# Performance work log

Measured on AMD Instinct MI355X. Metric: run time of the kernel, lower is better.

## Reference

```python
import jax, jax.numpy as jnp
import numpy as np

B, T, C = 2, 2048, 2048
N_HEAD, N_KV = 16, 2
D_HEAD = C // N_HEAD          # 128
R = N_HEAD // N_KV            # q heads per kv head = 8


def setup_inputs() -> dict:
    key = jax.random.key(0)
    ks = jax.random.split(key, 5)
    s = 0.02
    return {
        "x": jax.random.normal(ks[0], (B, T, C), dtype=jnp.float32),
        "Wq": jax.random.normal(ks[1], (C, C), dtype=jnp.float32) * s,
        "Wk": jax.random.normal(ks[2], (C, N_KV * D_HEAD), dtype=jnp.float32) * s,
        "Wv": jax.random.normal(ks[3], (C, N_KV * D_HEAD), dtype=jnp.float32) * s,
        "Wo": jax.random.normal(ks[4], (C, C), dtype=jnp.float32) * s,
    }


def reference(x, Wq, Wk, Wv, Wo):
    b, t, c = x.shape
    # projections (no bias per config.bias=False)
    q = (x @ Wq).reshape(b, t, N_KV, R, D_HEAD)        # group q heads by kv group
    k = (x @ Wk).reshape(b, t, N_KV, D_HEAD)
    v = (x @ Wv).reshape(b, t, N_KV, D_HEAD)
    scale = 1.0 / jnp.sqrt(jnp.float32(D_HEAD))
    # scores: [b, g(kv), r, tq, tk] -- broadcast kv heads instead of repeat_interleave
    att = jnp.einsum('btgrd,bsgd->bgrts', q, k) * scale
    causal = jnp.tril(jnp.ones((t, t), dtype=bool))
    att = jnp.where(causal, att, -jnp.inf)
    att = jax.nn.softmax(att, axis=-1)
    y = jnp.einsum('bgrts,bsgd->btgrd', att, v).reshape(b, t, c)
    return y @ Wo
```

## Files before the change

kernel.cpp:

```cpp
#include <hip/hip_runtime.h>
#include <stdint.h>

using bf16x8 = __attribute__((ext_vector_type(8))) __bf16;
using f32x4  = __attribute__((ext_vector_type(4))) float;

#define GLL(g, l) __builtin_amdgcn_global_load_lds(                                  \
    (const __attribute__((address_space(1))) void*)(g),                              \
    (__attribute__((address_space(3))) void*)(l), 16, 0, 0)

__device__ __forceinline__ unsigned short f2bf(float f) {
  unsigned u = __builtin_bit_cast(unsigned, f);
  u += 0x7FFF + ((u >> 16) & 1);
  return (unsigned short)(u >> 16);
}
__device__ __forceinline__ float bf2f(unsigned short u) {
  unsigned v = ((unsigned)u) << 16;
  return __builtin_bit_cast(float, v);
}

__global__ __launch_bounds__(256) void cast_kernel(const float* __restrict__ in,
                                                   unsigned short* __restrict__ out, int n4) {
  int i = blockIdx.x * 256 + threadIdx.x;
  if (i >= n4) return;
  float4 v = reinterpret_cast<const float4*>(in)[i];
  ushort4 o;
  o.x = f2bf(v.x); o.y = f2bf(v.y); o.z = f2bf(v.z); o.w = f2bf(v.w);
  reinterpret_cast<ushort4*>(out)[i] = o;
}

__global__ __launch_bounds__(256) void tcast_all_kernel(const float* __restrict__ Wq,
                                                        const float* __restrict__ Wk,
                                                        const float* __restrict__ Wv,
                                                        const float* __restrict__ Wo,
                                                        unsigned short* __restrict__ Wqkvt,
                                                        unsigned short* __restrict__ Wot) {
  __shared__ float T[64][65];
  const int y = blockIdx.y;
  const float* W;
  unsigned short* Wt;
  int N, n0;
  if (y < 32)      { W = Wq; Wt = Wqkvt;                          N = 2048; n0 = y * 64; }
  else if (y < 36) { W = Wk; Wt = Wqkvt + (size_t)2048 * 2048;    N = 256;  n0 = (y - 32) * 64; }
  else if (y < 40) { W = Wv; Wt = Wqkvt + (size_t)2304 * 2048;    N = 256;  n0 = (y - 36) * 64; }
  else             { W = Wo; Wt = Wot;                            N = 2048; n0 = (y - 40) * 64; }
  const int k0 = blockIdx.x * 64;
  const int t = threadIdx.x;
  const int r4 = t >> 6, c = t & 63;
#pragma unroll
  for (int p = 0; p < 16; ++p) {
    int r = p * 4 + r4;
    T[r][c] = W[(size_t)(k0 + r) * N + n0 + c];
  }
  __syncthreads();
#pragma unroll
  for (int p = 0; p < 16; ++p) {
    int r = p * 4 + r4;
    Wt[(size_t)(n0 + r) * 2048 + k0 + c] = f2bf(T[c][r]);
  }
}

__global__ __launch_bounds__(256) void tv_kernel(const unsigned short* __restrict__ V,
                                                 unsigned short* __restrict__ Vt) {
  __shared__ unsigned short T[64][68];
  const int t0 = blockIdx.x * 64;
  const int d0 = blockIdx.y * 64;
  const int t = threadIdx.x;
  const int r4 = t >> 6, c = t & 63;
#pragma unroll
  for (int p = 0; p < 16; ++p) {
    int r = p * 4 + r4;
    T[r][c] = V[(size_t)(t0 + r) * 2560 + 2304 + d0 + c];
  }
  __syncthreads();
  const int b = t0 >> 11;
  const int tl = t0 & 2047;
#pragma unroll
  for (int p = 0; p < 16; ++p) {
    int dr = p * 4 + r4;
    int dg = d0 + dr;
    int g = dg >> 7, dl = dg & 127;
    Vt[(size_t)((b * 2 + g) * 128 + dl) * 2048 + tl + c] = T[c][dr];
  }
}

template <bool FP32OUT>
__global__ __launch_bounds__(256) void gemm_bt_kernel(const unsigned short* __restrict__ A,
                                                      const unsigned short* __restrict__ Bt,
                                                      void* __restrict__ Cout,
                                                      int K, int lda, int ldb, int ldc,
                                                      float scale, int nscale) {
  __shared__ __align__(16) unsigned short As[128 * 64];
  __shared__ __align__(16) unsigned short Bs[128 * 64];
  const int m0 = blockIdx.x * 128, n0 = blockIdx.y * 128;
  const int t = threadIdx.x;
  const int w = t >> 6, lane = t & 63;
  const int l15 = lane & 15, quad = lane >> 4;
  const int wm = (w >> 1) * 64, wn = (w & 1) * 64;

  const int srow = lane >> 3;
  const int sgl = (lane & 7) ^ srow;

  f32x4 acc[4][4] = {};

  for (int k0 = 0; k0 < K; k0 += 64) {
    __syncthreads();
#pragma unroll
    for (int p = 0; p < 4; ++p) {
      int rowbase = p * 32 + w * 8;
      GLL(&A[(size_t)(m0 + rowbase + srow) * lda + k0 + sgl * 8], &As[rowbase * 64]);
      GLL(&Bt[(size_t)(n0 + rowbase + srow) * ldb + k0 + sgl * 8], &Bs[rowbase * 64]);
    }
    __syncthreads();
#pragma unroll
    for (int kk = 0; kk < 64; kk += 32) {
      const int kg = kk >> 3;
      const int phys = ((kg + quad) ^ (l15 & 7)) * 8;
      bf16x8 af[4], bfr[4];
#pragma unroll
      for (int mt = 0; mt < 4; ++mt)
        af[mt] = *reinterpret_cast<const bf16x8*>(&As[(wm + mt * 16 + l15) * 64 + phys]);
#pragma unroll
      for (int nt = 0; nt < 4; ++nt)
        bfr[nt] = *reinterpret_cast<const bf16x8*>(&Bs[(wn + nt * 16 + l15) * 64 + phys]);
#pragma unroll
      for (int mt = 0; mt < 4; ++mt)
#pragma unroll
        for (int nt = 0; nt < 4; ++nt)
          acc[mt][nt] = __builtin_amdgcn_mfma_f32_16x16x32_bf16(af[mt], bfr[nt], acc[mt][nt], 0, 0, 0);
    }
  }

  const float sc = (n0 < nscale) ? scale : 1.0f;
#pragma unroll
  for (int mt = 0; mt < 4; ++mt) {
#pragma unroll
    for (int reg = 0; reg < 4; ++reg) {
      int row = m0 + wm + mt * 16 + quad * 4 + reg;
#pragma unroll
      for (int nt = 0; nt < 4; ++nt) {
        int col = n0 + wn + nt * 16 + l15;
        float v = acc[mt][nt][reg] * sc;
        if (FP32OUT)
          reinterpret_cast<float*>(Cout)[(size_t)row * ldc + col] = v;
        else
          reinterpret_cast<unsigned short*>(Cout)[(size_t)row * ldc + col] = f2bf(v);
      }
    }
  }
}

#define LDQK 2560
__global__ __launch_bounds__(256, 4) void attn_kernel(const unsigned short* __restrict__ Q,
                                                      const unsigned short* __restrict__ Kg,
                                                      const unsigned short* __restrict__ Vt,
                                                      float* __restrict__ O0,
                                                      unsigned short* __restrict__ O1,
                                                      float* __restrict__ L) {
  __shared__ __align__(16) unsigned short Ks[2][32 * 128];
  __shared__ __align__(16) unsigned short Vs[2][128 * 32];
  __shared__ __align__(16) unsigned short Pw[4][16 * 40];

  const int s  = blockIdx.x;
  const int by = blockIdx.y;
  const int hh = blockIdx.z & 15;
  const int b  = blockIdx.z >> 4;
  const int g  = hh >> 3;
  const int t  = threadIdx.x;
  const int wg = t >> 6, lane = t & 63;
  const int l15 = lane & 15, quad = lane >> 4;

  const unsigned short* Kbase = Kg + (size_t)b * 2048 * LDQK + g * 128;
  const unsigned short* Vbase = Vt + (size_t)(b * 2 + g) * 128 * 2048;

  const int k_r = lane >> 4;
  const int k_g = lane & 15;
  const int v_r = lane >> 2;
  const int v_g = lane & 3;

  auto issueK = [&](int tile, int buf) {
    const unsigned short* kb = Kbase + (size_t)(tile * 32) * LDQK;
#pragma unroll
    for (int p = 0; p < 2; ++p) {
      int rowbase = p * 16 + wg * 4;
      int row = rowbase + k_r;
      int gl = k_g ^ (row & 15);
      GLL(&kb[(size_t)row * LDQK + gl * 8], &Ks[buf][rowbase * 128]);
    }
  };
  auto issueV = [&](int tile, int buf) {
    const unsigned short* vb = Vbase + tile * 32;
#pragma unroll
    for (int p = 0; p < 2; ++p) {
      int rowbase = p * 64 + wg * 16;
      int row = rowbase + v_r;
      int gl = v_g ^ (row & 3);
      GLL(&vb[(size_t)row * 2048 + gl * 8], &Vs[buf][rowbase * 32]);
    }
  };

  int pb = 0;
  issueK(s, 0);
  issueV(s, 0);

  for (int ph = 0; ph < 2; ++ph) {
    const int qt = ph ? (31 - by) : by;

    bf16x8 qf[4];
    {
      int qrow = qt * 64 + wg * 16 + l15;
      const unsigned short* qp = &Q[(size_t)(b * 2048 + qrow) * LDQK + hh * 128 + quad * 8];
#pragma unroll
      for (int dk = 0; dk < 4; ++dk)
        qf[dk] = *reinterpret_cast<const bf16x8*>(qp + dk * 32);
    }

    f32x4 o[8] = {};
    float l_run[4] = {};

    for (int j = 0; j <= qt; ++j) {
      const int tile = 2 * j + s;
      __syncthreads();
      const int cur = pb, nxt = pb ^ 1;

      if (j < qt) {
        issueK(tile + 2, nxt);
        issueV(tile + 2, nxt);
      } else if (ph == 0) {
        issueK(s, nxt);
        issueV(s, nxt);
      }

      f32x4 sc[2] = {};
#pragma unroll
      for (int nt = 0; nt < 2; ++nt) {
#pragma unroll
        for (int dk = 0; dk < 4; ++dk) {
          int phys = (dk * 4 + quad) ^ l15;
          bf16x8 kf = *reinterpret_cast<const bf16x8*>(&Ks[cur][(nt * 16 + l15) * 128 + phys * 8]);
          sc[nt] = __builtin_amdgcn_mfma_f32_16x16x32_bf16(qf[dk], kf, sc[nt], 0, 0, 0);
        }
      }
      if (j == qt) {
#pragma unroll
        for (int nt = 0; nt < 2; ++nt) {
          int kcol = tile * 32 + nt * 16 + l15;
#pragma unroll
          for (int reg = 0; reg < 4; ++reg) {
            int qr = qt * 64 + wg * 16 + quad * 4 + reg;
            if (kcol > qr) sc[nt][reg] = -1e30f;
          }
        }
      }
#pragma unroll
      for (int nt = 0; nt < 2; ++nt)
#pragma unroll
        for (int reg = 0; reg < 4; ++reg) {
          float p = __builtin_exp2f(__builtin_fmaf(sc[nt][reg], 1.44269504f, -23.08312064f));
          l_run[reg] += p;
          Pw[wg][(quad * 4 + reg) * 40 + nt * 16 + l15] = f2bf(p);
        }

      bf16x8 pf = *reinterpret_cast<const bf16x8*>(&Pw[wg][l15 * 40 + quad * 8]);
#pragma unroll
      for (int dt = 0; dt < 8; ++dt) {
        int phys = quad ^ (l15 & 3);
        bf16x8 vf = *reinterpret_cast<const bf16x8*>(&Vs[cur][(dt * 16 + l15) * 32 + phys * 8]);
        o[dt] = __builtin_amdgcn_mfma_f32_16x16x32_bf16(pf, vf, o[dt], 0, 0, 0);
      }
      pb ^= 1;
    }

#pragma unroll
    for (int off = 1; off <= 8; off <<= 1)
#pragma unroll
      for (int reg = 0; reg < 4; ++reg)
        l_run[reg] += __shfl_xor(l_run[reg], off);

#pragma unroll
    for (int reg = 0; reg < 4; ++reg) {
      int row = wg * 16 + quad * 4 + reg;
      size_t base = (size_t)(b * 2048 + qt * 64 + row) * 2048 + hh * 128;
      if (s == 0) {
#pragma unroll
        for (int dt = 0; dt < 8; ++dt)
          O0[base + dt * 16 + l15] = o[dt][reg];
      } else {
#pragma unroll
        for (int dt = 0; dt < 8; ++dt)
          O1[base + dt * 16 + l15] = f2bf(o[dt][reg]);
      }
      if (l15 == 0)
        L[(size_t)s * 65536 + (size_t)(b * 2048 + qt * 64 + row) * 16 + hh] = l_run[reg];
    }
  }
}

__global__ __launch_bounds__(256) void merge_kernel(const float* __restrict__ O0,
                                                    unsigned short* __restrict__ O1,
                                                    const float* __restrict__ L) {
  int i4 = blockIdx.x * 256 + threadIdx.x;
  int e = i4 << 2;
  int tr = e >> 11;
  int hh = (e >> 7) & 15;
  float l = L[tr * 16 + hh] + L[65536 + tr * 16 + hh];
  float inv = 1.0f / l;
  float4 a = reinterpret_cast<const float4*>(O0)[i4];
  ushort4 u = reinterpret_cast<const ushort4*>(O1)[i4];
  ushort4 r;
  r.x = f2bf((a.x + bf2f(u.x)) * inv);
  r.y = f2bf((a.y + bf2f(u.y)) * inv);
  r.z = f2bf((a.z + bf2f(u.z)) * inv);
  r.w = f2bf((a.w + bf2f(u.w)) * inv);
  reinterpret_cast<ushort4*>(O1)[i4] = r;
}

extern "C" void kernel_launch(void* const* d_in, const int* in_sizes, int n_in,
                              void* d_out, int out_size, void* d_ws, size_t ws_size,
                              hipStream_t stream) {
  const float* x  = (const float*)d_in[0];
  const float* Wq = (const float*)d_in[1];
  const float* Wk = (const float*)d_in[2];
  const float* Wv = (const float*)d_in[3];
  const float* Wo = (const float*)d_in[4];

  char* ws = (char*)d_ws;
  unsigned short* xb    = (unsigned short*)(ws + 0);
  unsigned short* Wqkvt = (unsigned short*)(ws + 16777216);
  unsigned short* Wot   = (unsigned short*)(ws + 27262976);
  unsigned short* QKVb  = (unsigned short*)(ws + 35651584);
  unsigned short* Vtb   = (unsigned short*)(ws + 56623104);
  float*          Lb    = (float*)(ws + 58720256);
  unsigned short* Yb    = xb;

  cast_kernel<<<8192, 256, 0, stream>>>(x, xb, 2097152);
  tcast_all_kernel<<<dim3(32, 72), 256, 0, stream>>>(Wq, Wk, Wv, Wo, Wqkvt, Wot);

  const float qscale = 0.08838834764831845f;
  gemm_bt_kernel<false><<<dim3(32, 20), 256, 0, stream>>>(xb, Wqkvt, QKVb,
                                                          2048, 2048, 2048, 2560, qscale, 2048);
  tv_kernel<<<dim3(64, 4), 256, 0, stream>>>(QKVb, Vtb);
  attn_kernel<<<dim3(2, 16, 32), 256, 0, stream>>>(QKVb, QKVb + 2048, Vtb,
                                                   (float*)d_out, Yb, Lb);
  merge_kernel<<<8192, 256, 0, stream>>>((const float*)d_out, Yb, Lb);
  gemm_bt_kernel<true><<<dim3(32, 16), 256, 0, stream>>>(Yb, Wot, d_out,
                                                         2048, 2048, 2048, 2048, 1.0f, 0);
}
```

Baseline: 288.3 us.

## Enlarge attention tiles to 256 query rows and 64-key blocks per workgroup

Each attention workgroup now processes 256 query rows (64 per wave) against 64-key K/V tiles, reusing each K/V fragment across four MFMA row tiles. This cuts LDS and global traffic per FLOP and reduces the grid to 256 workgroups with one block per CU. The partial output for split 0 is also stored as bf16 instead of fp32, halving that write and the merge read. The cost is very high register use and low occupancy, giving less latency hiding, plus slightly reduced precision in the partial sum.

```diff
diff --git a/kernel.cpp b/kernel.cpp
--- a/kernel.cpp
+++ b/kernel.cpp
@@ -150,18 +150,18 @@
 }
 
 #define LDQK 2560
-__global__ __launch_bounds__(256, 4) void attn_kernel(const unsigned short* __restrict__ Q,
+__global__ __launch_bounds__(256, 1) void attn_kernel(const unsigned short* __restrict__ Q,
                                                       const unsigned short* __restrict__ Kg,
                                                       const unsigned short* __restrict__ Vt,
-                                                      float* __restrict__ O0,
+                                                      unsigned short* __restrict__ O0,
                                                       unsigned short* __restrict__ O1,
                                                       float* __restrict__ L) {
-  __shared__ __align__(16) unsigned short Ks[2][32 * 128];
-  __shared__ __align__(16) unsigned short Vs[2][128 * 32];
-  __shared__ __align__(16) unsigned short Pw[4][16 * 40];
+  __shared__ __align__(16) unsigned short Ks[2][64 * 128];
+  __shared__ __align__(16) unsigned short Vs[2][128 * 64];
+  __shared__ __align__(16) unsigned short Pw[4][64 * 68];
 
   const int s  = blockIdx.x;
-  const int by = blockIdx.y;
+  const int bp = blockIdx.y;
   const int hh = blockIdx.z & 15;
   const int b  = blockIdx.z >> 4;
   const int g  = hh >> 3;
@@ -173,28 +173,26 @@
   const unsigned short* Vbase = Vt + (size_t)(b * 2 + g) * 128 * 2048;
 
   const int k_r = lane >> 4;
-  const int k_g = lane & 15;
-  const int v_r = lane >> 2;
-  const int v_g = lane & 3;
+  const int v_r = lane >> 3;
 
   auto issueK = [&](int tile, int buf) {
-    const unsigned short* kb = Kbase + (size_t)(tile * 32) * LDQK;
-#pragma unroll
-    for (int p = 0; p < 2; ++p) {
+    const unsigned short* kb = Kbase + (size_t)(tile * 64) * LDQK;
+#pragma unroll
+    for (int p = 0; p < 4; ++p) {
       int rowbase = p * 16 + wg * 4;
       int row = rowbase + k_r;
-      int gl = k_g ^ (row & 15);
+      int gl = (lane & 15) ^ (row & 15);
       GLL(&kb[(size_t)row * LDQK + gl * 8], &Ks[buf][rowbase * 128]);
     }
   };
   auto issueV = [&](int tile, int buf) {
-    const unsigned short* vb = Vbase + tile * 32;
-#pragma unroll
-    for (int p = 0; p < 2; ++p) {
-      int rowbase = p * 64 + wg * 16;
+    const unsigned short* vb = Vbase + tile * 64;
+#pragma unroll
+    for (int p = 0; p < 4; ++p) {
+      int rowbase = p * 32 + wg * 8;
       int row = rowbase + v_r;
-      int gl = v_g ^ (row & 3);
-      GLL(&vb[(size_t)row * 2048 + gl * 8], &Vs[buf][rowbase * 32]);
+      int gl = (lane & 7) ^ (row & 7);
+      GLL(&vb[(size_t)row * 2048 + gl * 8], &Vs[buf][rowbase * 64]);
     }
   };
 
@@ -203,26 +201,28 @@
   issueV(s, 0);
 
   for (int ph = 0; ph < 2; ++ph) {
-    const int qt = ph ? (31 - by) : by;
-
-    bf16x8 qf[4];
-    {
-      int qrow = qt * 64 + wg * 16 + l15;
+    const int qt = ph ? (7 - bp) : bp;
+
+    bf16x8 qf[4][4];
+#pragma unroll
+    for (int mi = 0; mi < 4; ++mi) {
+      int qrow = qt * 256 + wg * 64 + mi * 16 + l15;
       const unsigned short* qp = &Q[(size_t)(b * 2048 + qrow) * LDQK + hh * 128 + quad * 8];
 #pragma unroll
       for (int dk = 0; dk < 4; ++dk)
-        qf[dk] = *reinterpret_cast<const bf16x8*>(qp + dk * 32);
-    }
-
-    f32x4 o[8] = {};
-    float l_run[4] = {};
-
-    for (int j = 0; j <= qt; ++j) {
+        qf[mi][dk] = *reinterpret_cast<const bf16x8*>(qp + dk * 32);
+    }
+
+    f32x4 o[4][8] = {};
+    float l_run[4][4] = {};
+    const int nj = 2 * qt + 2;
+
+    for (int j = 0; j < nj; ++j) {
       const int tile = 2 * j + s;
       __syncthreads();
       const int cur = pb, nxt = pb ^ 1;
 
-      if (j < qt) {
+      if (j + 1 < nj) {
         issueK(tile + 2, nxt);
         issueV(tile + 2, nxt);
       } else if (ph == 0) {
@@ -230,72 +230,86 @@
         issueV(s, nxt);
       }
 
-      f32x4 sc[2] = {};
-#pragma unroll
-      for (int nt = 0; nt < 2; ++nt) {
+      f32x4 sc[4][4] = {};
+#pragma unroll
+      for (int nt = 0; nt < 4; ++nt) {
 #pragma unroll
         for (int dk = 0; dk < 4; ++dk) {
           int phys = (dk * 4 + quad) ^ l15;
           bf16x8 kf = *reinterpret_cast<const bf16x8*>(&Ks[cur][(nt * 16 + l15) * 128 + phys * 8]);
-          sc[nt] = __builtin_amdgcn_mfma_f32_16x16x32_bf16(qf[dk], kf, sc[nt], 0, 0, 0);
+#pragma unroll
+          for (int mi = 0; mi < 4; ++mi)
+            sc[mi][nt] = __builtin_amdgcn_mfma_f32_16x16x32_bf16(qf[mi][dk], kf, sc[mi][nt], 0, 0, 0);
         }
       }
-      if (j == qt) {
-#pragma unroll
-        for (int nt = 0; nt < 2; ++nt) {
-          int kcol = tile * 32 + nt * 16 + l15;
+      if (tile >= 4 * qt) {
+#pragma unroll
+        for (int mi = 0; mi < 4; ++mi)
+#pragma unroll
+          for (int nt = 0; nt < 4; ++nt) {
+            int kcol = tile * 64 + nt * 16 + l15;
+#pragma unroll
+            for (int reg = 0; reg < 4; ++reg) {
+              int qr = qt * 256 + wg * 64 + mi * 16 + quad * 4 + reg;
+              if (kcol > qr) sc[mi][nt][reg] = -1e30f;
+            }
+          }
+      }
+#pragma unroll
+      for (int mi = 0; mi < 4; ++mi)
+#pragma unroll
+        for (int nt = 0; nt < 4; ++nt)
 #pragma unroll
           for (int reg = 0; reg < 4; ++reg) {
-            int qr = qt * 64 + wg * 16 + quad * 4 + reg;
-            if (kcol > qr) sc[nt][reg] = -1e30f;
+            float p = __builtin_exp2f(__builtin_fmaf(sc[mi][nt][reg], 1.44269504f, -23.08312064f));
+            l_run[mi][reg] += p;
+            Pw[wg][(mi * 16 + quad * 4 + reg) * 68 + nt * 16 + l15] = f2bf(p);
           }
+
+#pragma unroll
+      for (int kk = 0; kk < 2; ++kk) {
+        const int kg = kk * 4;
+        bf16x8 pf[4];
+#pragma unroll
+        for (int mi = 0; mi < 4; ++mi)
+          pf[mi] = *reinterpret_cast<const bf16x8*>(&Pw[wg][(mi * 16 + l15) * 68 + kk * 32 + quad * 8]);
+#pragma unroll
+        for (int dt = 0; dt < 8; ++dt) {
+          int phys = (kg + quad) ^ (l15 & 7);
+          bf16x8 vf = *reinterpret_cast<const bf16x8*>(&Vs[cur][(dt * 16 + l15) * 64 + phys * 8]);
+#pragma unroll
+          for (int mi = 0; mi < 4; ++mi)
+            o[mi][dt] = __builtin_amdgcn_mfma_f32_16x16x32_bf16(pf[mi], vf, o[mi][dt], 0, 0, 0);
         }
       }
-#pragma unroll
-      for (int nt = 0; nt < 2; ++nt)
-#pragma unroll
-        for (int reg = 0; reg < 4; ++reg) {
-          float p = __builtin_exp2f(__builtin_fmaf(sc[nt][reg], 1.44269504f, -23.08312064f));
-          l_run[reg] += p;
-          Pw[wg][(quad * 4 + reg) * 40 + nt * 16 + l15] = f2bf(p);
-        }
-
-      bf16x8 pf = *reinterpret_cast<const bf16x8*>(&Pw[wg][l15 * 40 + quad * 8]);
-#pragma unroll
-      for (int dt = 0; dt < 8; ++dt) {
-        int phys = quad ^ (l15 & 3);
-        bf16x8 vf = *reinterpret_cast<const bf16x8*>(&Vs[cur][(dt * 16 + l15) * 32 + phys * 8]);
-        o[dt] = __builtin_amdgcn_mfma_f32_16x16x32_bf16(pf, vf, o[dt], 0, 0, 0);
-      }
       pb ^= 1;
     }
 
 #pragma unroll
     for (int off = 1; off <= 8; off <<= 1)
 #pragma unroll
-      for (int reg = 0; reg < 4; ++reg)
-        l_run[reg] += __shfl_xor(l_run[reg], off);
-
-#pragma unroll
-    for (int reg = 0; reg < 4; ++reg) {
-      int row = wg * 16 + quad * 4 + reg;
-      size_t base = (size_t)(b * 2048 + qt * 64 + row) * 2048 + hh * 128;
-      if (s == 0) {
+      for (int mi = 0; mi < 4; ++mi)
+#pragma unroll
+        for (int reg = 0; reg < 4; ++reg)
+          l_run[mi][reg] += __shfl_xor(l_run[mi][reg], off);
+
+    unsigned short* Op = s ? O1 : O0;
+#pragma unroll
+    for (int mi = 0; mi < 4; ++mi)
+#pragma unroll
+      for (int reg = 0; reg < 4; ++reg) {
+        int row = wg * 64 + mi * 16 + quad * 4 + reg;
+        size_t base = (size_t)(b * 2048 + qt * 256 + row) * 2048 + hh * 128;
 #pragma unroll
         for (int dt = 0; dt < 8; ++dt)
-          O0[base + dt * 16 + l15] = o[dt][reg];
-      } else {
-#pragma unroll
-        for (int dt = 0; dt < 8; ++dt)
-          O1[base + dt * 16 + l15] = f2bf(o[dt][reg]);
-      }
-      if (l15 == 0)
-        L[(size_t)s * 65536 + (size_t)(b * 2048 + qt * 64 + row) * 16 + hh] = l_run[reg];
-    }
-  }
-}
-
-__global__ __launch_bounds__(256) void merge_kernel(const float* __restrict__ O0,
+          Op[base + dt * 16 + l15] = f2bf(o[mi][dt][reg]);
+        if (l15 == 0)
+          L[(size_t)s * 65536 + (size_t)(b * 2048 + qt * 256 + row) * 16 + hh] = l_run[mi][reg];
+      }
+  }
+}
+
+__global__ __launch_bounds__(256) void merge_kernel(const unsigned short* __restrict__ O0,
                                                     unsigned short* __restrict__ O1,
                                                     const float* __restrict__ L) {
   int i4 = blockIdx.x * 256 + threadIdx.x;
@@ -304,13 +318,13 @@
   int hh = (e >> 7) & 15;
   float l = L[tr * 16 + hh] + L[65536 + tr * 16 + hh];
   float inv = 1.0f / l;
-  float4 a = reinterpret_cast<const float4*>(O0)[i4];
+  ushort4 a = reinterpret_cast<const ushort4*>(O0)[i4];
   ushort4 u = reinterpret_cast<const ushort4*>(O1)[i4];
   ushort4 r;
-  r.x = f2bf((a.x + bf2f(u.x)) * inv);
-  r.y = f2bf((a.y + bf2f(u.y)) * inv);
-  r.z = f2bf((a.z + bf2f(u.z)) * inv);
-  r.w = f2bf((a.w + bf2f(u.w)) * inv);
+  r.x = f2bf((bf2f(a.x) + bf2f(u.x)) * inv);
+  r.y = f2bf((bf2f(a.y) + bf2f(u.y)) * inv);
+  r.z = f2bf((bf2f(a.z) + bf2f(u.z)) * inv);
+  r.w = f2bf((bf2f(a.w) + bf2f(u.w)) * inv);
   reinterpret_cast<ushort4*>(O1)[i4] = r;
 }
 
@@ -339,9 +353,9 @@
   gemm_bt_kernel<false><<<dim3(32, 20), 256, 0, stream>>>(xb, Wqkvt, QKVb,
                                                           2048, 2048, 2048, 2560, qscale, 2048);
   tv_kernel<<<dim3(64, 4), 256, 0, stream>>>(QKVb, Vtb);
-  attn_kernel<<<dim3(2, 16, 32), 256, 0, stream>>>(QKVb, QKVb + 2048, Vtb,
-                                                   (float*)d_out, Yb, Lb);
-  merge_kernel<<<8192, 256, 0, stream>>>((const float*)d_out, Yb, Lb);
+  attn_kernel<<<dim3(2, 4, 32), 256, 0, stream>>>(QKVb, QKVb + 2048, Vtb,
+                                                  (unsigned short*)d_out, Yb, Lb);
+  merge_kernel<<<8192, 256, 0, stream>>>((const unsigned short*)d_out, Yb, Lb);
   gemm_bt_kernel<true><<<dim3(32, 16), 256, 0, stream>>>(Yb, Wot, d_out,
                                                          2048, 2048, 2048, 2048, 1.0f, 0);
 }
```

Result: slower. 306.7 us (+6.4%).
